# Optimization experiments

Hardware: AMD Instinct MI355X
Metric: run time of the kernel (lower is better)

## Reference

```python
import jax, jax.numpy as jnp
import numpy as np
from functools import partial

N_NODES = 10000
E_EDGES = 160000
SEQ = 32
IN_CH = 128
HID = 64
HEADS = 8
GRU_H = 256
NEG_SLOPE = 0.2


def setup_inputs() -> dict:
    key = jax.random.key(0)
    ks = jax.random.split(key, 24)
    x = jax.random.normal(ks[0], (SEQ, N_NODES, IN_CH), dtype=jnp.float32)
    edge_attr = jax.random.normal(ks[1], (E_EDGES, 3), dtype=jnp.float32)
    edge_src = jax.random.randint(ks[2], (E_EDGES,), 0, N_NODES, dtype=jnp.int32)
    # guarantee no self loops (PyG removes then re-adds them; we add them in reference)
    off = jax.random.randint(ks[3], (E_EDGES,), 1, N_NODES, dtype=jnp.int32)
    edge_dst = (edge_src + off) % N_NODES
    s = 0.05
    p = {}
    # gat1: in -> heads*hid
    p['gat1_wl'] = jax.random.normal(ks[4], (IN_CH, HEADS * HID)) * s
    p['gat1_wr'] = jax.random.normal(ks[5], (IN_CH, HEADS * HID)) * s
    p['gat1_we'] = jax.random.normal(ks[6], (3, HEADS * HID)) * s
    p['gat1_att'] = jax.random.normal(ks[7], (HEADS, HID)) * s
    p['gat1_b'] = jnp.zeros((HEADS * HID,), jnp.float32)
    # gat2: heads*hid -> 1*hid
    p['gat2_wl'] = jax.random.normal(ks[8], (HEADS * HID, HID)) * s
    p['gat2_wr'] = jax.random.normal(ks[9], (HEADS * HID, HID)) * s
    p['gat2_we'] = jax.random.normal(ks[10], (3, HID)) * s
    p['gat2_att'] = jax.random.normal(ks[11], (1, HID)) * s
    p['gat2_b'] = jnp.zeros((HID,), jnp.float32)
    # GRU layer 0, forward and backward directions (only layer 0 affects the output)
    p['gru_wih_f'] = jax.random.normal(ks[12], (3 * GRU_H, HID)) * s
    p['gru_whh_f'] = jax.random.normal(ks[13], (3 * GRU_H, GRU_H)) * s
    p['gru_bih_f'] = jnp.zeros((3 * GRU_H,), jnp.float32)
    p['gru_bhh_f'] = jnp.zeros((3 * GRU_H,), jnp.float32)
    p['gru_wih_b'] = jax.random.normal(ks[14], (3 * GRU_H, HID)) * s
    p['gru_whh_b'] = jax.random.normal(ks[15], (3 * GRU_H, GRU_H)) * s
    p['gru_bih_b'] = jnp.zeros((3 * GRU_H,), jnp.float32)
    p['gru_bhh_b'] = jnp.zeros((3 * GRU_H,), jnp.float32)
    p['fc_w'] = jax.random.normal(ks[16], (33, 2 * GRU_H)) * s
    p['fc_b'] = jnp.zeros((33,), jnp.float32)
    return dict(x=x, edge_attr=edge_attr, edge_src=edge_src, edge_dst=edge_dst, **p)


def _gatv2(x, src, dst, e_emb, wl, wr, att, b, n_nodes):
    # x: [N, F_in]; e_emb: [E_full, H, C]; att: [H, C]
    H, C = att.shape
    xl = (x @ wl).reshape(n_nodes, H, C)
    xr = (x @ wr).reshape(n_nodes, H, C)
    m = jax.nn.leaky_relu(xl[src] + xr[dst] + e_emb, NEG_SLOPE)  # [E, H, C]
    logits = jnp.einsum('ehc,hc->eh', m, att)                    # [E, H]
    mx = jax.ops.segment_max(logits, dst, num_segments=n_nodes)
    ex = jnp.exp(logits - mx[dst])
    den = jax.ops.segment_sum(ex, dst, num_segments=n_nodes)
    alpha = ex / den[dst]
    out = jax.ops.segment_sum(alpha[:, :, None] * xl[src], dst, num_segments=n_nodes)
    return out.reshape(n_nodes, H * C) + b


def _gru_scan(seq, wih, whh, bih, bhh):
    # seq: [T, N, F]; returns final hidden [N, GRU_H]
    Hh = whh.shape[1]
    def cell(h, x_t):
        gi = x_t @ wih.T + bih
        gh = h @ whh.T + bhh
        ir, iz, inn = jnp.split(gi, 3, axis=-1)
        hr, hz, hn = jnp.split(gh, 3, axis=-1)
        r = jax.nn.sigmoid(ir + hr)
        z = jax.nn.sigmoid(iz + hz)
        n = jnp.tanh(inn + r * hn)
        h = (1.0 - z) * n + z * h
        return h, None
    h0 = jnp.zeros((seq.shape[1], Hh), seq.dtype)
    hT, _ = jax.lax.scan(cell, h0, seq)
    return hT


def reference(x, edge_attr, edge_src, edge_dst,
              gat1_wl, gat1_wr, gat1_we, gat1_att, gat1_b,
              gat2_wl, gat2_wr, gat2_we, gat2_att, gat2_b,
              gru_wih_f, gru_whh_f, gru_bih_f, gru_bhh_f,
              gru_wih_b, gru_whh_b, gru_bih_b, gru_bhh_b,
              fc_w, fc_b):
    T, N, _ = x.shape
    E = edge_src.shape[0]
    loop = jnp.arange(N, dtype=edge_src.dtype)
    src = jnp.concatenate([edge_src, loop])
    dst = jnp.concatenate([edge_dst, loop])
    # self-loop edge attr = mean of incoming edge attrs (PyG fill_value='mean')
    deg = jax.ops.segment_sum(jnp.ones((E,), x.dtype), edge_dst, num_segments=N)
    loop_attr = jax.ops.segment_sum(edge_attr, edge_dst, num_segments=N) / jnp.maximum(deg, 1.0)[:, None]
    ea = jnp.concatenate([edge_attr, loop_attr], axis=0)  # [E+N, 3]
    e1 = (ea @ gat1_we).reshape(-1, HEADS, HID)
    e2 = (ea @ gat2_we).reshape(-1, 1, HID)

    @jax.checkpoint
    def step(carry, x_t):
        h1 = jax.nn.elu(_gatv2(x_t, src, dst, e1, gat1_wl, gat1_wr, gat1_att, gat1_b, N))
        h2 = jax.nn.elu(_gatv2(h1, src, dst, e2, gat2_wl, gat2_wr, gat2_att, gat2_b, N))
        return carry, h2

    _, emb = jax.lax.scan(step, 0, x)  # [T, N, HID]

    # torch code uses h_n[0] (layer-0 fwd final) and h_n[1] (layer-0 bwd final);
    # deeper GRU layers do not influence the output.
    hf = _gru_scan(emb, gru_wih_f, gru_whh_f, gru_bih_f, gru_bhh_f)
    hb = _gru_scan(emb[::-1], gru_wih_b, gru_whh_b, gru_bih_b, gru_bhh_b)
    comb = jnp.concatenate([hf, hb], axis=1)           # [N, 512]
    g = jnp.mean(comb, axis=0, keepdims=True)          # [1, 512]
    return g @ fc_w.T + fc_b                           # [1, 33]
```

## Files before the change

### kernel.cpp

```cpp
#include <hip/hip_runtime.h>

#define T_SEQ   32
#define N_NODES 10000
#define E_EDGES 160000
#define EF      (E_EDGES + N_NODES)
#define IN_CH   128
#define HID     64
#define HEADS   8
#define HC      512
#define GRU_H   256
#define G3      768

typedef __attribute__((ext_vector_type(8))) short short8;
typedef __attribute__((ext_vector_type(4))) float f32x4;
typedef unsigned short ushort_t;

__device__ __forceinline__ float wave_reduce_sum(float v){
#pragma unroll
  for (int off = 32; off; off >>= 1) v += __shfl_xor(v, off, 64);
  return v;
}

__device__ __forceinline__ ushort_t f2bf(float v){
  unsigned u = __float_as_uint(v);
  unsigned r = u + 0x7FFFu + ((u >> 16) & 1u);
  return (ushort_t)(r >> 16);
}
__device__ __forceinline__ float bf2f(ushort_t b){
  return __uint_as_float(((unsigned)b) << 16);
}

__device__ __forceinline__ void async_cp16(const void* g, void* l){
  __builtin_amdgcn_global_load_lds((const __attribute__((address_space(1))) void*)g,
                                   (__attribute__((address_space(3))) void*)l, 16, 0, 0);
}


__global__ __launch_bounds__(256)
void deg_loop_kernel(const int* __restrict__ edst, const float* __restrict__ eattr,
                     int* __restrict__ deg, float* __restrict__ lsum){
  int e = blockIdx.x * 256 + threadIdx.x;
  if (e < E_EDGES){
    int d = edst[e];
    atomicAdd(&deg[d], 1);
    atomicAdd(&lsum[d*3+0], eattr[e*3+0]);
    atomicAdd(&lsum[d*3+1], eattr[e*3+1]);
    atomicAdd(&lsum[d*3+2], eattr[e*3+2]);
  }
}

__global__ __launch_bounds__(256)
void loop_div_kernel(const int* __restrict__ deg, const float* __restrict__ lsum,
                     float* __restrict__ lattr){
  int n = blockIdx.x * 256 + threadIdx.x;
  if (n < N_NODES){
    float d = fmaxf((float)deg[n], 1.0f);
    lattr[n*3+0] = lsum[n*3+0] / d;
    lattr[n*3+1] = lsum[n*3+1] / d;
    lattr[n*3+2] = lsum[n*3+2] / d;
  }
}

__global__ __launch_bounds__(256)
void scan_rowptr_kernel(const int* __restrict__ deg, int* __restrict__ row_ptr){
  __shared__ int sums[256];
  __shared__ int base[256];
  int tid = threadIdx.x;
  const int CH = 40;
  int start = tid * CH;
  int s = 0;
  for (int k = 0; k < CH; k++){
    int n = start + k;
    if (n < N_NODES) s += deg[n];
  }
  sums[tid] = s;
  __syncthreads();
  if (tid == 0){
    int acc = 0;
    for (int i = 0; i < 256; i++){ base[i] = acc; acc += sums[i]; }
  }
  __syncthreads();
  int acc = base[tid];
  for (int k = 0; k < CH; k++){
    int n = start + k;
    if (n < N_NODES){ row_ptr[n] = acc; acc += deg[n]; }
    else if (n == N_NODES){ row_ptr[n] = acc; }
  }
}

__global__ __launch_bounds__(256)
void csr_fill_kernel(const int* __restrict__ edst, const int* __restrict__ row_ptr,
                     int* __restrict__ cursor, int* __restrict__ col){
  int e = blockIdx.x * 256 + threadIdx.x;
  if (e < E_EDGES){
    int d = edst[e];
    int pos = row_ptr[d] + atomicAdd(&cursor[d], 1);
    col[pos] = e;
  }
}

__global__ __launch_bounds__(256)
void build_emeta(const float* __restrict__ eattr, const float* __restrict__ lattr,
                 const int* __restrict__ esrc, float4* __restrict__ emeta){
  int e = blockIdx.x * 256 + threadIdx.x;
  if (e < E_EDGES){
    emeta[e] = make_float4(eattr[e*3], eattr[e*3+1], eattr[e*3+2], __int_as_float(esrc[e]));
  } else if (e < EF){
    int n = e - E_EDGES;
    emeta[e] = make_float4(lattr[n*3], lattr[n*3+1], lattr[n*3+2], __int_as_float(n));
  }
}


__global__ __launch_bounds__(256)
void split_arr4(const float4* __restrict__ src, ushort4* __restrict__ hi,
                ushort4* __restrict__ lo, long n4){
  long idx = (long)blockIdx.x * 256 + threadIdx.x;
  if (idx < n4){
    float4 v = src[idx];
    float vv[4] = {v.x, v.y, v.z, v.w};
    ushort4 h, l;
    ushort_t* hp = (ushort_t*)&h; ushort_t* lp = (ushort_t*)&l;
#pragma unroll
    for (int i = 0; i < 4; i++){
      ushort_t hh = f2bf(vv[i]);
      hp[i] = hh; lp[i] = f2bf(vv[i] - bf2f(hh));
    }
    hi[idx] = h; lo[idx] = l;
  }
}

__global__ __launch_bounds__(256)
void split_w_gat1(const float* __restrict__ wl, const float* __restrict__ wr,
                  ushort_t* __restrict__ hi, ushort_t* __restrict__ lo){
  int idx = blockIdx.x * 256 + threadIdx.x;
  if (idx >= 1024 * 128) return;
  int n = idx >> 7, k = idx & 127;
  float v = (n < 512) ? wl[k * 512 + n] : wr[k * 512 + (n - 512)];
  ushort_t h = f2bf(v);
  hi[idx] = h; lo[idx] = f2bf(v - bf2f(h));
}

__global__ __launch_bounds__(256)
void split_w_gat2(const float* __restrict__ wl, const float* __restrict__ wr,
                  ushort_t* __restrict__ hi, ushort_t* __restrict__ lo){
  int idx = blockIdx.x * 256 + threadIdx.x;
  if (idx >= 128 * 512) return;
  int n = idx >> 9, k = idx & 511;
  float v = (n < 64) ? wl[k * 64 + n] : wr[k * 64 + (n - 64)];
  ushort_t h = f2bf(v);
  hi[idx] = h; lo[idx] = f2bf(v - bf2f(h));
}

__global__ __launch_bounds__(256)
void pack_w_gru(const float* __restrict__ wih, const float* __restrict__ whh,
                ushort_t* __restrict__ hi, ushort_t* __restrict__ lo){
  int idx = blockIdx.x * 256 + threadIdx.x;
  if (idx >= 4 * 10 * 192 * 32) return;
  int kk = idx & 31;
  int r  = (idx >> 5) % 192;
  int kc = (idx >> 5) / 192 % 10;
  int jt = idx / (32 * 192 * 10);
  int g = r >> 6, jj = r & 63;
  int wrow = g * 256 + jt * 64 + jj;
  int k = kc * 32 + kk;
  float v = (k < 64) ? wih[wrow * 64 + k] : whh[wrow * 256 + (k - 64)];
  ushort_t h = f2bf(v);
  hi[idx] = h; lo[idx] = f2bf(v - bf2f(h));
}


__global__ __launch_bounds__(256)
void gemm_nolds(const ushort_t* __restrict__ Ah, const ushort_t* __restrict__ Al,
                const ushort_t* __restrict__ Bh, const ushort_t* __restrict__ Bl,
                float* __restrict__ C, int M, int K, int N){
  int tid = threadIdx.x;
  int w = tid >> 6, lane = tid & 63;
  int m16 = lane & 15, quad = lane >> 4;
  int n0 = (blockIdx.y * 4 + w) * 64;
  if (n0 >= N) return;
  int m0 = blockIdx.x * 32;

  f32x4 acc[2][4];
#pragma unroll
  for (int i = 0; i < 2; i++)
#pragma unroll
    for (int j = 0; j < 4; j++) acc[i][j] = (f32x4){0,0,0,0};

  int ar0 = m0 + m16;      if (ar0 >= M) ar0 = M - 1;
  int ar1 = m0 + 16 + m16; if (ar1 >= M) ar1 = M - 1;
  const ushort_t* Ah0 = Ah + (size_t)ar0 * K + quad * 8;
  const ushort_t* Al0 = Al + (size_t)ar0 * K + quad * 8;
  const ushort_t* Ah1 = Ah + (size_t)ar1 * K + quad * 8;
  const ushort_t* Al1 = Al + (size_t)ar1 * K + quad * 8;

  for (int k0 = 0; k0 < K; k0 += 32){
    short8 a_h[2], a_l[2];
    a_h[0] = *(const short8*)(Ah0 + k0); a_l[0] = *(const short8*)(Al0 + k0);
    a_h[1] = *(const short8*)(Ah1 + k0); a_l[1] = *(const short8*)(Al1 + k0);
#pragma unroll
    for (int nt = 0; nt < 4; nt++){
      size_t boff = (size_t)(n0 + nt * 16 + m16) * K + k0 + quad * 8;
      short8 b_h = *(const short8*)(Bh + boff);
      short8 b_l = *(const short8*)(Bl + boff);
#pragma unroll
      for (int mt = 0; mt < 2; mt++){
        acc[mt][nt] = __builtin_amdgcn_mfma_f32_16x16x32_bf16(a_h[mt], b_h, acc[mt][nt],0,0,0);
        acc[mt][nt] = __builtin_amdgcn_mfma_f32_16x16x32_bf16(a_h[mt], b_l, acc[mt][nt],0,0,0);
        acc[mt][nt] = __builtin_amdgcn_mfma_f32_16x16x32_bf16(a_l[mt], b_h, acc[mt][nt],0,0,0);
      }
    }
  }
#pragma unroll
  for (int mt = 0; mt < 2; mt++){
    int row = m0 + mt * 16 + quad * 4;
#pragma unroll
    for (int nt = 0; nt < 4; nt++){
      int cc = n0 + nt * 16 + m16;
#pragma unroll
      for (int r4 = 0; r4 < 4; r4++){
        if (row + r4 < M) C[(size_t)(row + r4) * N + cc] = acc[mt][nt][r4];
      }
    }
  }
}


struct GruArgs {
  const ushort_t *EtH[2], *EtL[2];
  const ushort_t *WpH[2], *WpL[2];
  const float    *BIH[2], *BHH[2];
  const ushort_t *HinH[2],*HinL[2];
  ushort_t *HoutH[2], *HoutL[2];
};

#define GRU_STAGE(AH, AL, ASTRIDE, ACOL)                                       \
  {                                                                            \
    _Pragma("unroll")                                                          \
    for (int pass = 0; pass < 2; pass++){                                      \
      int chunk = pass * 256 + tid;                 \
      int row = chunk >> 2, c = (chunk & 3) * 8;                               \
      int anode = m0 + row; if (anode >= N_NODES) anode = N_NODES - 1;         \
      async_cp16(AH + (size_t)anode * ASTRIDE + (ACOL) + c, &Ah_s[chunk * 8]); \
      async_cp16(AL + (size_t)anode * ASTRIDE + (ACOL) + c, &Al_s[chunk * 8]); \
    }                                                                          \
    const ushort_t* bh = WpH + ((size_t)jt * 10 + kc) * 6144;                  \
    const ushort_t* bl = WpL + ((size_t)jt * 10 + kc) * 6144;                  \
    _Pragma("unroll")                                                          \
    for (int pass = 0; pass < 3; pass++){                                      \
      int chunk = pass * 256 + tid;                 \
      async_cp16(bh + chunk * 8, &Bh_s[chunk * 8]);                            \
      async_cp16(bl + chunk * 8, &Bl_s[chunk * 8]);                            \
    }                                                                          \
  }

#define GRU_COMPUTE(NTGT)                                                      \
  {                                                                            \
    short8 a_h[4], a_l[4];                                                     \
    _Pragma("unroll")                                                          \
    for (int mt = 0; mt < 4; mt++){                                            \
      int r = wm * 64 + mt * 16 + m16;                                         \
      a_h[mt] = *(const short8*)&Ah_s[r * 32 + quad * 8];                      \
      a_l[mt] = *(const short8*)&Al_s[r * 32 + quad * 8];                      \
    }                                                                          \
    _Pragma("unroll")                                                          \
    for (int g = 0; g < 3; g++){                                               \
      int tgt = (g < 2) ? g : (NTGT);                                          \
      _Pragma("unroll")                                                        \
      for (int nt = 0; nt < 2; nt++){                                          \
        int r = g * 64 + wn * 32 + nt * 16 + m16;                              \
        short8 b_h = *(const short8*)&Bh_s[r * 32 + quad * 8];                 \
        short8 b_l = *(const short8*)&Bl_s[r * 32 + quad * 8];                 \
        _Pragma("unroll")                                                      \
        for (int mt = 0; mt < 4; mt++){                                        \
          acc[tgt][mt][nt] = __builtin_amdgcn_mfma_f32_16x16x32_bf16(a_h[mt], b_h, acc[tgt][mt][nt],0,0,0); \
          acc[tgt][mt][nt] = __builtin_amdgcn_mfma_f32_16x16x32_bf16(a_h[mt], b_l, acc[tgt][mt][nt],0,0,0); \
          acc[tgt][mt][nt] = __builtin_amdgcn_mfma_f32_16x16x32_bf16(a_l[mt], b_h, acc[tgt][mt][nt],0,0,0); \
        }                                                                      \
      }                                                                        \
    }                                                                          \
  }

__global__ __launch_bounds__(256, 2)
void gru_step(GruArgs ga){
  int dir = blockIdx.z;
  const ushort_t* EtH  = ga.EtH[dir];  const ushort_t* EtL  = ga.EtL[dir];
  const ushort_t* WpH  = ga.WpH[dir];  const ushort_t* WpL  = ga.WpL[dir];
  const float*    BIH  = ga.BIH[dir];  const float*    BHH  = ga.BHH[dir];
  const ushort_t* HinH = ga.HinH[dir]; const ushort_t* HinL = ga.HinL[dir];
  ushort_t* HoutH = ga.HoutH[dir];     ushort_t* HoutL = ga.HoutL[dir];

  __shared__ __align__(16) short Ah_s[128 * 32];
  __shared__ __align__(16) short Al_s[128 * 32];
  __shared__ __align__(16) short Bh_s[192 * 32];
  __shared__ __align__(16) short Bl_s[192 * 32];

  int tid = threadIdx.x;
  int w = tid >> 6, lane = tid & 63;
  int wm = w >> 1, wn = w & 1;
  int m16 = lane & 15, quad = lane >> 4;
  int m0 = blockIdx.x * 128;
  int jt = blockIdx.y;
  int j0 = jt * 64;

  f32x4 acc[4][4][2];
#pragma unroll
  for (int g = 0; g < 4; g++)
#pragma unroll
    for (int i = 0; i < 4; i++)
#pragma unroll
      for (int j = 0; j < 2; j++) acc[g][i][j] = (f32x4){0,0,0,0};

  for (int kc = 0; kc < 2; kc++){
    if (kc) __syncthreads();
    int k0 = kc * 32;
    GRU_STAGE(EtH, EtL, 64, k0)
    __syncthreads();
    GRU_COMPUTE(2)
  }
  for (int kc = 2; kc < 10; kc++){
    __syncthreads();
    int k0 = kc * 32;
    GRU_STAGE(HinH, HinL, 256, k0 - 64)
    __syncthreads();
    GRU_COMPUTE(3)
  }

#pragma unroll
  for (int mt = 0; mt < 4; mt++){
    int row = m0 + wm * 64 + mt * 16 + quad * 4;
#pragma unroll
    for (int nt = 0; nt < 2; nt++){
      int j = j0 + wn * 32 + nt * 16 + m16;
      float br  = BIH[j] + BHH[j];
      float bz  = BIH[GRU_H + j] + BHH[GRU_H + j];
      float bni = BIH[2*GRU_H + j];
      float bnh = BHH[2*GRU_H + j];
#pragma unroll
      for (int r4 = 0; r4 < 4; r4++){
        int node = row + r4;
        if (node < N_NODES){
          float rr = 1.f / (1.f + __expf(-(acc[0][mt][nt][r4] + br)));
          float zz = 1.f / (1.f + __expf(-(acc[1][mt][nt][r4] + bz)));
          float nn = tanhf(acc[2][mt][nt][r4] + bni + rr * (acc[3][mt][nt][r4] + bnh));
          size_t hidx = (size_t)node * GRU_H + j;
          float hold = bf2f(HinH[hidx]) + bf2f(HinL[hidx]);
          float hv = (1.f - zz) * nn + zz * hold;
          ushort_t hh = f2bf(hv);
          HoutH[hidx] = hh;
          HoutL[hidx] = f2bf(hv - bf2f(hh));
        }
      }
    }
  }
}


__device__ __forceinline__ void gat1_half(float4 xl, float4 xr,
                                          float a0, float a1, float a2,
                                          float4 we0, float4 we1, float4 we2,
                                          float4 at, bool valid,
                                          float& den, float4& acc){
  float vx = xl.x + xr.x + a0*we0.x + a1*we1.x + a2*we2.x;
  float vy = xl.y + xr.y + a0*we0.y + a1*we1.y + a2*we2.y;
  float vz = xl.z + xr.z + a0*we0.z + a1*we1.z + a2*we2.z;
  float vw = xl.w + xr.w + a0*we0.w + a1*we1.w + a2*we2.w;
  vx = fmaxf(vx, 0.2f*vx); vy = fmaxf(vy, 0.2f*vy);
  vz = fmaxf(vz, 0.2f*vz); vw = fmaxf(vw, 0.2f*vw);
  float pm = vx*at.x + vy*at.y + vz*at.z + vw*at.w;
  pm += __shfl_xor(pm, 1, 64); pm += __shfl_xor(pm, 2, 64);
  pm += __shfl_xor(pm, 4, 64); pm += __shfl_xor(pm, 8, 64);
  float wgt = valid ? __expf(pm) : 0.f;
  den += wgt;
  acc.x += wgt * xl.x; acc.y += wgt * xl.y;
  acc.z += wgt * xl.z; acc.w += wgt * xl.w;
}

__global__ __launch_bounds__(256)
void gat1_fused(const float* __restrict__ xlr, const float4* __restrict__ emeta,
                const int* __restrict__ row_ptr, const int* __restrict__ col,
                const float* __restrict__ we, const float* __restrict__ att,
                const float* __restrict__ bias,
                ushort_t* __restrict__ outh, ushort_t* __restrict__ outl){
  int n = (blockIdx.x * 256 + threadIdx.x) >> 6;
  int lane = threadIdx.x & 63;
  if (n >= N_NODES) return;
  int ch0 = lane * 4;
  int ch1 = 256 + lane * 4;

  float4 att0 = *(const float4*)&att[ch0];
  float4 att1 = *(const float4*)&att[ch1];
  float4 we00 = *(const float4*)&we[ch0],        we01 = *(const float4*)&we[ch1];
  float4 we10 = *(const float4*)&we[512 + ch0],  we11 = *(const float4*)&we[512 + ch1];
  float4 we20 = *(const float4*)&we[1024 + ch0], we21 = *(const float4*)&we[1024 + ch1];
  const float* xrow_n = xlr + (size_t)n * 1024;
  float4 xr0 = *(const float4*)&xrow_n[512 + ch0];
  float4 xr1 = *(const float4*)&xrow_n[512 + ch1];

  float den0 = 0.f, den1 = 0.f;
  float4 acc0 = make_float4(0,0,0,0), acc1 = make_float4(0,0,0,0);
  int beg = row_ptr[n], end = row_ptr[n + 1];

  for (int p = beg - 1; p < end; p += 2){
    int c0 = (p >= beg) ? col[p] : (E_EDGES + n);
    bool v1 = (p + 1 < end);
    int c1 = v1 ? col[p + 1] : c0;
    float4 mt0 = emeta[c0];
    float4 mt1 = emeta[c1];
    const float* xp0 = xlr + (size_t)__float_as_int(mt0.w) * 1024;
    const float* xp1 = xlr + (size_t)__float_as_int(mt1.w) * 1024;
    float4 xa0 = *(const float4*)&xp0[ch0];
    float4 xa1 = *(const float4*)&xp0[ch1];
    float4 xb0 = *(const float4*)&xp1[ch0];
    float4 xb1 = *(const float4*)&xp1[ch1];
    gat1_half(xa0, xr0, mt0.x, mt0.y, mt0.z, we00, we10, we20, att0, true, den0, acc0);
    gat1_half(xa1, xr1, mt0.x, mt0.y, mt0.z, we01, we11, we21, att1, true, den1, acc1);
    gat1_half(xb0, xr0, mt1.x, mt1.y, mt1.z, we00, we10, we20, att0, v1, den0, acc0);
    gat1_half(xb1, xr1, mt1.x, mt1.y, mt1.z, we01, we11, we21, att1, v1, den1, acc1);
  }

  float4 b0 = *(const float4*)&bias[ch0];
  float4 b1 = *(const float4*)&bias[ch1];
  float id0 = 1.f / den0, id1 = 1.f / den1;
  float o[8];
  o[0] = acc0.x*id0 + b0.x; o[1] = acc0.y*id0 + b0.y;
  o[2] = acc0.z*id0 + b0.z; o[3] = acc0.w*id0 + b0.w;
  o[4] = acc1.x*id1 + b1.x; o[5] = acc1.y*id1 + b1.y;
  o[6] = acc1.z*id1 + b1.z; o[7] = acc1.w*id1 + b1.w;
  ushort4 h0, h1v, l0, l1v;
  ushort_t* hp0 = (ushort_t*)&h0; ushort_t* hp1 = (ushort_t*)&h1v;
  ushort_t* lp0 = (ushort_t*)&l0; ushort_t* lp1 = (ushort_t*)&l1v;
#pragma unroll
  for (int i = 0; i < 8; i++){
    float v = o[i];
    v = v > 0.f ? v : (__expf(v) - 1.f);
    ushort_t hh = f2bf(v);
    ushort_t ll = f2bf(v - bf2f(hh));
    if (i < 4){ hp0[i] = hh; lp0[i] = ll; } else { hp1[i-4] = hh; lp1[i-4] = ll; }
  }
  *(ushort4*)&outh[(size_t)n * 512 + ch0] = h0;
  *(ushort4*)&outh[(size_t)n * 512 + ch1] = h1v;
  *(ushort4*)&outl[(size_t)n * 512 + ch0] = l0;
  *(ushort4*)&outl[(size_t)n * 512 + ch1] = l1v;
}


__global__ __launch_bounds__(256)
void gat2_fused(const float* __restrict__ xlr, const float4* __restrict__ emeta,
                const int* __restrict__ row_ptr, const int* __restrict__ col,
                const float* __restrict__ we, const float* __restrict__ att,
                const float* __restrict__ bias,
                ushort_t* __restrict__ outh, ushort_t* __restrict__ outl){
  int n = (blockIdx.x * 256 + threadIdx.x) >> 6;
  int lane = threadIdx.x & 63;
  if (n >= N_NODES) return;
  int g = lane >> 4;
  int c4 = (lane & 15) * 4;

  float4 attq = *(const float4*)&att[c4];
  float4 we0q = *(const float4*)&we[c4];
  float4 we1q = *(const float4*)&we[64 + c4];
  float4 we2q = *(const float4*)&we[128 + c4];
  float4 xr4  = *(const float4*)&xlr[(size_t)n * 128 + 64 + c4];

  float den = 0.f;
  float4 acc = make_float4(0,0,0,0);
  int beg = row_ptr[n], end = row_ptr[n + 1];

  for (int p0 = beg - 1; p0 < end; p0 += 4){
    int pp = p0 + g;
    bool valid = pp < end;
    int s = n; float a0 = 0.f, a1 = 0.f, a2 = 0.f;
    if (valid){
      float4 mt = (pp < beg) ? emeta[E_EDGES + n] : emeta[col[pp]];
      a0 = mt.x; a1 = mt.y; a2 = mt.z; s = __float_as_int(mt.w);
    }
    float4 xl4 = *(const float4*)&xlr[(size_t)s * 128 + c4];
    float vx = xl4.x + xr4.x + a0*we0q.x + a1*we1q.x + a2*we2q.x;
    float vy = xl4.y + xr4.y + a0*we0q.y + a1*we1q.y + a2*we2q.y;
    float vz = xl4.z + xr4.z + a0*we0q.z + a1*we1q.z + a2*we2q.z;
    float vw = xl4.w + xr4.w + a0*we0q.w + a1*we1q.w + a2*we2q.w;
    vx = fmaxf(vx, 0.2f*vx); vy = fmaxf(vy, 0.2f*vy);
    vz = fmaxf(vz, 0.2f*vz); vw = fmaxf(vw, 0.2f*vw);
    float pm = vx*attq.x + vy*attq.y + vz*attq.z + vw*attq.w;
    pm += __shfl_xor(pm, 1, 64); pm += __shfl_xor(pm, 2, 64);
    pm += __shfl_xor(pm, 4, 64); pm += __shfl_xor(pm, 8, 64);
    float wgt = valid ? __expf(pm) : 0.f;
    den += wgt;
    acc.x += wgt * xl4.x; acc.y += wgt * xl4.y;
    acc.z += wgt * xl4.z; acc.w += wgt * xl4.w;
  }
#pragma unroll
  for (int off = 16; off <= 32; off <<= 1){
    den   += __shfl_xor(den, off, 64);
    acc.x += __shfl_xor(acc.x, off, 64);
    acc.y += __shfl_xor(acc.y, off, 64);
    acc.z += __shfl_xor(acc.z, off, 64);
    acc.w += __shfl_xor(acc.w, off, 64);
  }
  if (g == 0){
    float4 bq = *(const float4*)&bias[c4];
    float id = 1.f / den;
    float o[4];
    o[0] = acc.x*id + bq.x; o[1] = acc.y*id + bq.y;
    o[2] = acc.z*id + bq.z; o[3] = acc.w*id + bq.w;
    ushort4 hv, lv;
    ushort_t* hp = (ushort_t*)&hv; ushort_t* lp = (ushort_t*)&lv;
#pragma unroll
    for (int i = 0; i < 4; i++){
      float v = o[i];
      v = v > 0.f ? v : (__expf(v) - 1.f);
      ushort_t hh = f2bf(v);
      hp[i] = hh; lp[i] = f2bf(v - bf2f(hh));
    }
    *(ushort4*)&outh[(size_t)n * 64 + c4] = hv;
    *(ushort4*)&outl[(size_t)n * 64 + c4] = lv;
  }
}


__global__ __launch_bounds__(256)
void mean_kernel(const ushort_t* __restrict__ hfh, const ushort_t* __restrict__ hfl,
                 const ushort_t* __restrict__ hbh, const ushort_t* __restrict__ hbl,
                 float* __restrict__ g){
  int k = threadIdx.x;
  int n0 = blockIdx.x * 50;
  int n1 = n0 + 50; if (n1 > N_NODES) n1 = N_NODES;
  float sf = 0.f, sb = 0.f;
  for (int n = n0; n < n1; n++){
    size_t i = (size_t)n * GRU_H + k;
    sf += bf2f(hfh[i]) + bf2f(hfl[i]);
    sb += bf2f(hbh[i]) + bf2f(hbl[i]);
  }
  atomicAdd(&g[k], sf);
  atomicAdd(&g[GRU_H + k], sb);
}

__global__ __launch_bounds__(64)
void fc_kernel(const float* __restrict__ g, const float* __restrict__ W,
               const float* __restrict__ b, float* __restrict__ out){
  int j = blockIdx.x;
  int lane = threadIdx.x;
  float s = 0.f;
  for (int k = lane; k < 2 * GRU_H; k += 64) s += g[k] * W[j * (2 * GRU_H) + k];
  s = wave_reduce_sum(s);
  if (lane == 0) out[j] = b[j] + s * (1.0f / N_NODES);
}


extern "C" void kernel_launch(void* const* d_in, const int* in_sizes, int n_in,
                              void* d_out, int out_size, void* d_ws, size_t ws_size,
                              hipStream_t stream){
  const float* x     = (const float*)d_in[0];
  const float* eattr = (const float*)d_in[1];
  const int*   esrc  = (const int*)  d_in[2];
  const int*   edst  = (const int*)  d_in[3];
  const float* g1_wl = (const float*)d_in[4];
  const float* g1_wr = (const float*)d_in[5];
  const float* g1_we = (const float*)d_in[6];
  const float* g1_att= (const float*)d_in[7];
  const float* g1_b  = (const float*)d_in[8];
  const float* g2_wl = (const float*)d_in[9];
  const float* g2_wr = (const float*)d_in[10];
  const float* g2_we = (const float*)d_in[11];
  const float* g2_att= (const float*)d_in[12];
  const float* g2_b  = (const float*)d_in[13];
  const float* wih_f = (const float*)d_in[14];
  const float* whh_f = (const float*)d_in[15];
  const float* bih_f = (const float*)d_in[16];
  const float* bhh_f = (const float*)d_in[17];
  const float* wih_b = (const float*)d_in[18];
  const float* whh_b = (const float*)d_in[19];
  const float* bih_b = (const float*)d_in[20];
  const float* bhh_b = (const float*)d_in[21];
  const float* fc_w  = (const float*)d_in[22];
  const float* fc_b  = (const float*)d_in[23];
  float* out = (float*)d_out;

  float* ws = (float*)d_ws;
  size_t o = 0;
  auto alloc = [&](size_t nfloats) -> float* {
    float* p = ws + o; o += (nfloats + 3) & ~(size_t)3; return p;
  };
  const size_t XTOT = (size_t)T_SEQ * N_NODES * IN_CH;
  ushort_t* xh   = (ushort_t*)alloc(XTOT / 2);
  ushort_t* xlo  = (ushort_t*)alloc(XTOT / 2);
  float* xlr1    = alloc((size_t)N_NODES * 1024);
  ushort_t* h1h  = (ushort_t*)alloc((size_t)N_NODES * 512 / 2 + 4);
  ushort_t* h1l  = (ushort_t*)alloc((size_t)N_NODES * 512 / 2 + 4);
  const size_t ETOT = (size_t)T_SEQ * N_NODES * HID;
  ushort_t* embh = (ushort_t*)alloc(ETOT / 2);
  ushort_t* embl = (ushort_t*)alloc(ETOT / 2);
  const size_t HTOT = (size_t)N_NODES * GRU_H;
  ushort_t* hbuf[8];
  for (int i = 0; i < 8; i++) hbuf[i] = (ushort_t*)alloc(HTOT / 2 + 4);
  float* lsum  = alloc((size_t)N_NODES * 3);
  float* lattr = alloc((size_t)N_NODES * 3);
  float* gmean = alloc(512);
  float4* emeta = (float4*)alloc((size_t)EF * 4);
  ushort_t* W1h = (ushort_t*)alloc(1024*128/2);
  ushort_t* W1l = (ushort_t*)alloc(1024*128/2);
  ushort_t* W2h = (ushort_t*)alloc(128*512/2);
  ushort_t* W2l = (ushort_t*)alloc(128*512/2);
  const size_t WPK = 4 * 10 * 192 * 32;
  ushort_t* WpFh = (ushort_t*)alloc(WPK/2);
  ushort_t* WpFl = (ushort_t*)alloc(WPK/2);
  ushort_t* WpBh = (ushort_t*)alloc(WPK/2);
  ushort_t* WpBl = (ushort_t*)alloc(WPK/2);
  int* deg     = (int*)alloc(N_NODES + 4);
  int* row_ptr = (int*)alloc(N_NODES + 4);
  int* cursor  = (int*)alloc(N_NODES + 4);
  int* col     = (int*)alloc(E_EDGES + 4);
  float* xlr2 = xlr1;

  hipMemsetAsync(deg,    0, N_NODES * sizeof(int), stream);
  hipMemsetAsync(cursor, 0, N_NODES * sizeof(int), stream);
  hipMemsetAsync(lsum,   0, (size_t)N_NODES * 3 * sizeof(float), stream);
  hipMemsetAsync(gmean,  0, 512 * sizeof(float), stream);
  hipMemsetAsync(hbuf[0], 0, HTOT * sizeof(ushort_t), stream);
  hipMemsetAsync(hbuf[1], 0, HTOT * sizeof(ushort_t), stream);
  hipMemsetAsync(hbuf[4], 0, HTOT * sizeof(ushort_t), stream);
  hipMemsetAsync(hbuf[5], 0, HTOT * sizeof(ushort_t), stream);

  deg_loop_kernel<<<(E_EDGES + 255)/256, 256, 0, stream>>>(edst, eattr, deg, lsum);
  loop_div_kernel<<<(N_NODES + 255)/256, 256, 0, stream>>>(deg, lsum, lattr);
  scan_rowptr_kernel<<<1, 256, 0, stream>>>(deg, row_ptr);
  csr_fill_kernel<<<(E_EDGES + 255)/256, 256, 0, stream>>>(edst, row_ptr, cursor, col);
  build_emeta<<<(EF + 255)/256, 256, 0, stream>>>(eattr, lattr, esrc, emeta);
  split_arr4<<<(int)(XTOT / 4 / 256), 256, 0, stream>>>(
      (const float4*)x, (ushort4*)xh, (ushort4*)xlo, (long)(XTOT / 4));
  split_w_gat1<<<(1024*128 + 255)/256, 256, 0, stream>>>(g1_wl, g1_wr, W1h, W1l);
  split_w_gat2<<<(128*512 + 255)/256, 256, 0, stream>>>(g2_wl, g2_wr, W2h, W2l);
  pack_w_gru<<<(int)((WPK + 255)/256), 256, 0, stream>>>(wih_f, whh_f, WpFh, WpFl);
  pack_w_gru<<<(int)((WPK + 255)/256), 256, 0, stream>>>(wih_b, whh_b, WpBh, WpBl);

  const int MB32  = (N_NODES + 31) / 32;
  const int MB128 = (N_NODES + 127) / 128;
  const int NODE_BLOCKS = (N_NODES + 3) / 4;
  for (int t = 0; t < T_SEQ; t++){
    const ushort_t* xth = xh  + (size_t)t * N_NODES * IN_CH;
    const ushort_t* xtl = xlo + (size_t)t * N_NODES * IN_CH;
    gemm_nolds<<<dim3(MB32, 4), 256, 0, stream>>>(xth, xtl, W1h, W1l, xlr1,
                                                  N_NODES, IN_CH, 1024);
    gat1_fused<<<NODE_BLOCKS, 256, 0, stream>>>(
        xlr1, emeta, row_ptr, col, g1_we, g1_att, g1_b, h1h, h1l);
    gemm_nolds<<<dim3(MB32, 1), 128, 0, stream>>>(h1h, h1l, W2h, W2l, xlr2,
                                                  N_NODES, HC, 128);
    gat2_fused<<<NODE_BLOCKS, 256, 0, stream>>>(
        xlr2, emeta, row_ptr, col, g2_we, g2_att, g2_b,
        embh + (size_t)t * N_NODES * HID, embl + (size_t)t * N_NODES * HID);
  }

  {
    int fin = 0, bin = 4;
    for (int s = 0; s < T_SEQ; s++){
      int fo = fin ^ 2, bo = bin ^ 2;
      GruArgs ga;
      ga.EtH[0] = embh + (size_t)s * N_NODES * HID;
      ga.EtL[0] = embl + (size_t)s * N_NODES * HID;
      ga.EtH[1] = embh + (size_t)(T_SEQ - 1 - s) * N_NODES * HID;
      ga.EtL[1] = embl + (size_t)(T_SEQ - 1 - s) * N_NODES * HID;
      ga.WpH[0] = WpFh; ga.WpL[0] = WpFl; ga.WpH[1] = WpBh; ga.WpL[1] = WpBl;
      ga.BIH[0] = bih_f; ga.BHH[0] = bhh_f; ga.BIH[1] = bih_b; ga.BHH[1] = bhh_b;
      ga.HinH[0] = hbuf[fin];   ga.HinL[0] = hbuf[fin+1];
      ga.HinH[1] = hbuf[bin];   ga.HinL[1] = hbuf[bin+1];
      ga.HoutH[0] = hbuf[fo];   ga.HoutL[0] = hbuf[fo+1];
      ga.HoutH[1] = hbuf[bo];   ga.HoutL[1] = hbuf[bo+1];
      gru_step<<<dim3(MB128, 4, 2), 256, 0, stream>>>(ga);
      fin = fo; bin = bo;
    }
  }

  mean_kernel<<<(N_NODES + 49)/50, 256, 0, stream>>>(hbuf[0], hbuf[1], hbuf[4], hbuf[5], gmean);
  fc_kernel<<<33, 64, 0, stream>>>(gmean, fc_w, fc_b, out);
}
```

Baseline: 7.251 ms.

## Double-buffer GRU step LDS tiles and XOR-swizzle shared memory layout

The GRU step kernel now keeps two LDS buffers for the A (input/hidden) and B (weight) tiles. It prefetches the next K-chunk while MFMAs run on the current one, which removes one of the two barriers per chunk. Shared-memory chunk indices are also XOR-swizzled on both store and load to cut bank conflicts on the 16-byte fragment reads. LDS use per block doubles to about 80KB, which leaves little headroom for two blocks per CU. Overlap also depends on the async copy and wait semantics lining up with the remaining barriers.

New measurement: 7.422 ms. 1.02x slower.

```diff
diff --git a/kernel.cpp b/kernel.cpp
--- a/kernel.cpp
+++ b/kernel.cpp
@@ -234,34 +234,37 @@
   ushort_t *HoutH[2], *HoutL[2];
 };
 
-#define GRU_STAGE(AH, AL, ASTRIDE, ACOL)                                       \
+#define GRU_STAGE(BB, AH, AL, ASTRIDE, ACOL, KC)                               \
   {                                                                            \
     _Pragma("unroll")                                                          \
     for (int pass = 0; pass < 2; pass++){                                      \
-      int chunk = pass * 256 + tid;                 \
-      int row = chunk >> 2, c = (chunk & 3) * 8;                               \
+      int ch = pass * 256 + tid;             \
+      int lch = ch ^ ((ch >> 3) & 7);              \
+      int row = lch >> 2, c = (lch & 3) * 8;                                   \
       int anode = m0 + row; if (anode >= N_NODES) anode = N_NODES - 1;         \
-      async_cp16(AH + (size_t)anode * ASTRIDE + (ACOL) + c, &Ah_s[chunk * 8]); \
-      async_cp16(AL + (size_t)anode * ASTRIDE + (ACOL) + c, &Al_s[chunk * 8]); \
+      async_cp16(AH + (size_t)anode * ASTRIDE + (ACOL) + c, &Ah_s[BB][ch * 8]);\
+      async_cp16(AL + (size_t)anode * ASTRIDE + (ACOL) + c, &Al_s[BB][ch * 8]);\
     }                                                                          \
-    const ushort_t* bh = WpH + ((size_t)jt * 10 + kc) * 6144;                  \
-    const ushort_t* bl = WpL + ((size_t)jt * 10 + kc) * 6144;                  \
+    const ushort_t* bh = WpH + ((size_t)jt * 10 + (KC)) * 6144;                \
+    const ushort_t* bl = WpL + ((size_t)jt * 10 + (KC)) * 6144;                \
     _Pragma("unroll")                                                          \
     for (int pass = 0; pass < 3; pass++){                                      \
-      int chunk = pass * 256 + tid;                 \
-      async_cp16(bh + chunk * 8, &Bh_s[chunk * 8]);                            \
-      async_cp16(bl + chunk * 8, &Bl_s[chunk * 8]);                            \
+      int ch = pass * 256 + tid;             \
+      int lch = ch ^ ((ch >> 3) & 7);                                          \
+      async_cp16(bh + lch * 8, &Bh_s[BB][ch * 8]);                             \
+      async_cp16(bl + lch * 8, &Bl_s[BB][ch * 8]);                             \
     }                                                                          \
   }
 
-#define GRU_COMPUTE(NTGT)                                                      \
+#define GRU_COMPUTE(BB, NTGT)                                                  \
   {                                                                            \
     short8 a_h[4], a_l[4];                                                     \
     _Pragma("unroll")                                                          \
     for (int mt = 0; mt < 4; mt++){                                            \
       int r = wm * 64 + mt * 16 + m16;                                         \
-      a_h[mt] = *(const short8*)&Ah_s[r * 32 + quad * 8];                      \
-      a_l[mt] = *(const short8*)&Al_s[r * 32 + quad * 8];                      \
+      int so = ((r * 4 + quad) ^ ((r >> 1) & 7)) * 8;                          \
+      a_h[mt] = *(const short8*)&Ah_s[BB][so];                                 \
+      a_l[mt] = *(const short8*)&Al_s[BB][so];                                 \
     }                                                                          \
     _Pragma("unroll")                                                          \
     for (int g = 0; g < 3; g++){                                               \
@@ -269,8 +272,9 @@
       _Pragma("unroll")                                                        \
       for (int nt = 0; nt < 2; nt++){                                          \
         int r = g * 64 + wn * 32 + nt * 16 + m16;                              \
-        short8 b_h = *(const short8*)&Bh_s[r * 32 + quad * 8];                 \
-        short8 b_l = *(const short8*)&Bl_s[r * 32 + quad * 8];                 \
+        int so = ((r * 4 + quad) ^ ((r >> 1) & 7)) * 8;                        \
+        short8 b_h = *(const short8*)&Bh_s[BB][so];                            \
+        short8 b_l = *(const short8*)&Bl_s[BB][so];                            \
         _Pragma("unroll")                                                      \
         for (int mt = 0; mt < 4; mt++){                                        \
           acc[tgt][mt][nt] = __builtin_amdgcn_mfma_f32_16x16x32_bf16(a_h[mt], b_h, acc[tgt][mt][nt],0,0,0); \
@@ -290,10 +294,10 @@
   const ushort_t* HinH = ga.HinH[dir]; const ushort_t* HinL = ga.HinL[dir];
   ushort_t* HoutH = ga.HoutH[dir];     ushort_t* HoutL = ga.HoutL[dir];
 
-  __shared__ __align__(16) short Ah_s[128 * 32];
-  __shared__ __align__(16) short Al_s[128 * 32];
-  __shared__ __align__(16) short Bh_s[192 * 32];
-  __shared__ __align__(16) short Bl_s[192 * 32];
+  __shared__ __align__(16) short Ah_s[2][128 * 32];
+  __shared__ __align__(16) short Al_s[2][128 * 32];
+  __shared__ __align__(16) short Bh_s[2][192 * 32];
+  __shared__ __align__(16) short Bl_s[2][192 * 32];
 
   int tid = threadIdx.x;
   int w = tid >> 6, lane = tid & 63;
@@ -311,20 +315,20 @@
 #pragma unroll
       for (int j = 0; j < 2; j++) acc[g][i][j] = (f32x4){0,0,0,0};
 
-  for (int kc = 0; kc < 2; kc++){
-    if (kc) __syncthreads();
-    int k0 = kc * 32;
-    GRU_STAGE(EtH, EtL, 64, k0)
+  GRU_STAGE(0, EtH, EtL, 64, 0, 0)
+  __syncthreads();
+  GRU_STAGE(1, EtH, EtL, 64, 32, 1)
+  GRU_COMPUTE(0, 2)
+  __syncthreads();
+  GRU_STAGE(0, HinH, HinL, 256, 0, 2)
+  GRU_COMPUTE(1, 2)
+  __syncthreads();
+  for (int kc = 2; kc < 9; kc++){
+    GRU_STAGE((kc + 1) & 1, HinH, HinL, 256, (kc - 1) * 32, kc + 1)
+    GRU_COMPUTE(kc & 1, 3)
     __syncthreads();
-    GRU_COMPUTE(2)
-  }
-  for (int kc = 2; kc < 10; kc++){
-    __syncthreads();
-    int k0 = kc * 32;
-    GRU_STAGE(HinH, HinL, 256, k0 - 64)
-    __syncthreads();
-    GRU_COMPUTE(3)
-  }
+  }
+  GRU_COMPUTE(1, 3)
 
 #pragma unroll
   for (int mt = 0; mt < 4; mt++){
```

## Replace LDS-staged GRU step with direct-global-load MFMA kernel on smaller tiles

Applied to the files above, without the earlier changes.

The GRU step kernel no longer stages A (embeddings/hidden state) and B (packed weights) tiles through LDS with async copies and barriers. Fragments are loaded directly from global memory into registers. The node tile shrinks from 128 to 64 rows with launch bounds raised to 4 blocks per SM, doubling the grid for more occupancy and wave-level parallelism. A 'first' flag skips the hidden-state half of the GEMM and the zeroing memsets on step 0. The trade is that loads lose LDS reuse across waves and rely on cache, so global traffic per FLOP rises.

Measured after the change: 8.236 ms. 13.6% more time.

```diff
diff --git a/kernel.cpp b/kernel.cpp
--- a/kernel.cpp
+++ b/kernel.cpp
@@ -28,11 +28,6 @@
 }
 __device__ __forceinline__ float bf2f(ushort_t b){
   return __uint_as_float(((unsigned)b) << 16);
-}
-
-__device__ __forceinline__ void async_cp16(const void* g, void* l){
-  __builtin_amdgcn_global_load_lds((const __attribute__((address_space(1))) void*)g,
-                                   (__attribute__((address_space(3))) void*)l, 16, 0, 0);
 }
 
 
@@ -232,47 +227,28 @@
   const float    *BIH[2], *BHH[2];
   const ushort_t *HinH[2],*HinL[2];
   ushort_t *HoutH[2], *HoutL[2];
+  int first;
 };
 
-#define GRU_STAGE(AH, AL, ASTRIDE, ACOL)                                       \
+#define GRUN_STEP(KC, NTGT, AH0, AL0, AH1, AL1, KOFF)                          \
   {                                                                            \
-    _Pragma("unroll")                                                          \
-    for (int pass = 0; pass < 2; pass++){                                      \
-      int chunk = pass * 256 + tid;                 \
-      int row = chunk >> 2, c = (chunk & 3) * 8;                               \
-      int anode = m0 + row; if (anode >= N_NODES) anode = N_NODES - 1;         \
-      async_cp16(AH + (size_t)anode * ASTRIDE + (ACOL) + c, &Ah_s[chunk * 8]); \
-      async_cp16(AL + (size_t)anode * ASTRIDE + (ACOL) + c, &Al_s[chunk * 8]); \
-    }                                                                          \
-    const ushort_t* bh = WpH + ((size_t)jt * 10 + kc) * 6144;                  \
-    const ushort_t* bl = WpL + ((size_t)jt * 10 + kc) * 6144;                  \
-    _Pragma("unroll")                                                          \
-    for (int pass = 0; pass < 3; pass++){                                      \
-      int chunk = pass * 256 + tid;                 \
-      async_cp16(bh + chunk * 8, &Bh_s[chunk * 8]);                            \
-      async_cp16(bl + chunk * 8, &Bl_s[chunk * 8]);                            \
-    }                                                                          \
-  }
-
-#define GRU_COMPUTE(NTGT)                                                      \
-  {                                                                            \
-    short8 a_h[4], a_l[4];                                                     \
-    _Pragma("unroll")                                                          \
-    for (int mt = 0; mt < 4; mt++){                                            \
-      int r = wm * 64 + mt * 16 + m16;                                         \
-      a_h[mt] = *(const short8*)&Ah_s[r * 32 + quad * 8];                      \
-      a_l[mt] = *(const short8*)&Al_s[r * 32 + quad * 8];                      \
-    }                                                                          \
+    short8 a_h[2], a_l[2];                                                     \
+    a_h[0] = *(const short8*)((AH0) + (KOFF));                                 \
+    a_l[0] = *(const short8*)((AL0) + (KOFF));                                 \
+    a_h[1] = *(const short8*)((AH1) + (KOFF));                                 \
+    a_l[1] = *(const short8*)((AL1) + (KOFF));                                 \
+    const ushort_t* bh = WBh + (size_t)(KC) * 6144;                            \
+    const ushort_t* bl = WBl + (size_t)(KC) * 6144;                            \
     _Pragma("unroll")                                                          \
     for (int g = 0; g < 3; g++){                                               \
       int tgt = (g < 2) ? g : (NTGT);                                          \
       _Pragma("unroll")                                                        \
       for (int nt = 0; nt < 2; nt++){                                          \
         int r = g * 64 + wn * 32 + nt * 16 + m16;                              \
-        short8 b_h = *(const short8*)&Bh_s[r * 32 + quad * 8];                 \
-        short8 b_l = *(const short8*)&Bl_s[r * 32 + quad * 8];                 \
+        short8 b_h = *(const short8*)(bh + r * 32 + quad * 8);                 \
+        short8 b_l = *(const short8*)(bl + r * 32 + quad * 8);                 \
         _Pragma("unroll")                                                      \
-        for (int mt = 0; mt < 4; mt++){                                        \
+        for (int mt = 0; mt < 2; mt++){                                        \
           acc[tgt][mt][nt] = __builtin_amdgcn_mfma_f32_16x16x32_bf16(a_h[mt], b_h, acc[tgt][mt][nt],0,0,0); \
           acc[tgt][mt][nt] = __builtin_amdgcn_mfma_f32_16x16x32_bf16(a_h[mt], b_l, acc[tgt][mt][nt],0,0,0); \
           acc[tgt][mt][nt] = __builtin_amdgcn_mfma_f32_16x16x32_bf16(a_l[mt], b_h, acc[tgt][mt][nt],0,0,0); \
@@ -281,8 +257,8 @@
     }                                                                          \
   }
 
-__global__ __launch_bounds__(256, 2)
-void gru_step(GruArgs ga){
+__global__ __launch_bounds__(256, 4)
+void gru_nolds(GruArgs ga){
   int dir = blockIdx.z;
   const ushort_t* EtH  = ga.EtH[dir];  const ushort_t* EtL  = ga.EtL[dir];
   const ushort_t* WpH  = ga.WpH[dir];  const ushort_t* WpL  = ga.WpL[dir];
@@ -290,45 +266,47 @@
   const ushort_t* HinH = ga.HinH[dir]; const ushort_t* HinL = ga.HinL[dir];
   ushort_t* HoutH = ga.HoutH[dir];     ushort_t* HoutL = ga.HoutL[dir];
 
-  __shared__ __align__(16) short Ah_s[128 * 32];
-  __shared__ __align__(16) short Al_s[128 * 32];
-  __shared__ __align__(16) short Bh_s[192 * 32];
-  __shared__ __align__(16) short Bl_s[192 * 32];
-
   int tid = threadIdx.x;
   int w = tid >> 6, lane = tid & 63;
   int wm = w >> 1, wn = w & 1;
   int m16 = lane & 15, quad = lane >> 4;
-  int m0 = blockIdx.x * 128;
+  int m0 = blockIdx.x * 64;
   int jt = blockIdx.y;
   int j0 = jt * 64;
 
-  f32x4 acc[4][4][2];
+  f32x4 acc[4][2][2];
 #pragma unroll
   for (int g = 0; g < 4; g++)
 #pragma unroll
-    for (int i = 0; i < 4; i++)
+    for (int i = 0; i < 2; i++)
 #pragma unroll
       for (int j = 0; j < 2; j++) acc[g][i][j] = (f32x4){0,0,0,0};
 
-  for (int kc = 0; kc < 2; kc++){
-    if (kc) __syncthreads();
-    int k0 = kc * 32;
-    GRU_STAGE(EtH, EtL, 64, k0)
-    __syncthreads();
-    GRU_COMPUTE(2)
-  }
-  for (int kc = 2; kc < 10; kc++){
-    __syncthreads();
-    int k0 = kc * 32;
-    GRU_STAGE(HinH, HinL, 256, k0 - 64)
-    __syncthreads();
-    GRU_COMPUTE(3)
-  }
-
-#pragma unroll
-  for (int mt = 0; mt < 4; mt++){
-    int row = m0 + wm * 64 + mt * 16 + quad * 4;
+  int ar0 = m0 + wm * 32 + m16;      if (ar0 >= N_NODES) ar0 = N_NODES - 1;
+  int ar1 = m0 + wm * 32 + 16 + m16; if (ar1 >= N_NODES) ar1 = N_NODES - 1;
+
+  const ushort_t* EA0h = EtH + (size_t)ar0 * 64 + quad * 8;
+  const ushort_t* EA0l = EtL + (size_t)ar0 * 64 + quad * 8;
+  const ushort_t* EA1h = EtH + (size_t)ar1 * 64 + quad * 8;
+  const ushort_t* EA1l = EtL + (size_t)ar1 * 64 + quad * 8;
+  const ushort_t* HA0h = HinH + (size_t)ar0 * 256 + quad * 8;
+  const ushort_t* HA0l = HinL + (size_t)ar0 * 256 + quad * 8;
+  const ushort_t* HA1h = HinH + (size_t)ar1 * 256 + quad * 8;
+  const ushort_t* HA1l = HinL + (size_t)ar1 * 256 + quad * 8;
+  const ushort_t* WBh = WpH + (size_t)jt * 10 * 6144;
+  const ushort_t* WBl = WpL + (size_t)jt * 10 * 6144;
+
+  GRUN_STEP(0, 2, EA0h, EA0l, EA1h, EA1l, 0)
+  GRUN_STEP(1, 2, EA0h, EA0l, EA1h, EA1l, 32)
+  if (!ga.first){
+    for (int kc = 2; kc < 10; kc++){
+      GRUN_STEP(kc, 3, HA0h, HA0l, HA1h, HA1l, (kc - 2) * 32)
+    }
+  }
+
+#pragma unroll
+  for (int mt = 0; mt < 2; mt++){
+    int row = m0 + wm * 32 + mt * 16 + quad * 4;
 #pragma unroll
     for (int nt = 0; nt < 2; nt++){
       int j = j0 + wn * 32 + nt * 16 + m16;
@@ -344,7 +322,7 @@
           float zz = 1.f / (1.f + __expf(-(acc[1][mt][nt][r4] + bz)));
           float nn = tanhf(acc[2][mt][nt][r4] + bni + rr * (acc[3][mt][nt][r4] + bnh));
           size_t hidx = (size_t)node * GRU_H + j;
-          float hold = bf2f(HinH[hidx]) + bf2f(HinL[hidx]);
+          float hold = ga.first ? 0.f : (bf2f(HinH[hidx]) + bf2f(HinL[hidx]));
           float hv = (1.f - zz) * nn + zz * hold;
           ushort_t hh = f2bf(hv);
           HoutH[hidx] = hh;
@@ -617,10 +595,6 @@
   hipMemsetAsync(cursor, 0, N_NODES * sizeof(int), stream);
   hipMemsetAsync(lsum,   0, (size_t)N_NODES * 3 * sizeof(float), stream);
   hipMemsetAsync(gmean,  0, 512 * sizeof(float), stream);
-  hipMemsetAsync(hbuf[0], 0, HTOT * sizeof(ushort_t), stream);
-  hipMemsetAsync(hbuf[1], 0, HTOT * sizeof(ushort_t), stream);
-  hipMemsetAsync(hbuf[4], 0, HTOT * sizeof(ushort_t), stream);
-  hipMemsetAsync(hbuf[5], 0, HTOT * sizeof(ushort_t), stream);
 
   deg_loop_kernel<<<(E_EDGES + 255)/256, 256, 0, stream>>>(edst, eattr, deg, lsum);
   loop_div_kernel<<<(N_NODES + 255)/256, 256, 0, stream>>>(deg, lsum, lattr);
@@ -635,7 +609,7 @@
   pack_w_gru<<<(int)((WPK + 255)/256), 256, 0, stream>>>(wih_b, whh_b, WpBh, WpBl);
 
   const int MB32  = (N_NODES + 31) / 32;
-  const int MB128 = (N_NODES + 127) / 128;
+  const int MB64  = (N_NODES + 63) / 64;
   const int NODE_BLOCKS = (N_NODES + 3) / 4;
   for (int t = 0; t < T_SEQ; t++){
     const ushort_t* xth = xh  + (size_t)t * N_NODES * IN_CH;
@@ -666,7 +640,8 @@
       ga.HinH[1] = hbuf[bin];   ga.HinL[1] = hbuf[bin+1];
       ga.HoutH[0] = hbuf[fo];   ga.HoutL[0] = hbuf[fo+1];
       ga.HoutH[1] = hbuf[bo];   ga.HoutL[1] = hbuf[bo+1];
-      gru_step<<<dim3(MB128, 4, 2), 256, 0, stream>>>(ga);
+      ga.first = (s == 0) ? 1 : 0;
+      gru_nolds<<<dim3(MB64, 4, 2), 256, 0, stream>>>(ga);
       fin = fo; bin = bo;
     }
   }
```
